# Kernel optimization log

Hardware: AMD Instinct MI355X
Metric: run time of the kernel (lower is better)

The kernel has to match this reference:

```python
import jax, jax.numpy as jnp
import numpy as np

N_NODES = 100000
N_EDGES = 1600000
C = 64          # in = hidden = out channels
L = 3           # num_layers
BN_EPS = 1e-5


def setup_inputs() -> dict:
    key = jax.random.key(0)
    ks = jax.random.split(key, 16)
    x = jax.random.normal(ks[0], (N_NODES, C), dtype=jnp.float32)
    edge_index = jax.random.randint(ks[1], (2, N_EDGES), 0, N_NODES, dtype=jnp.int32)
    s = 1.0 / np.sqrt(C)
    # Stacked per-layer parameters (all layers are C->C).
    # Linear weights stored as [in, out] (i.e. torch weight transposed).
    W1 = jax.random.normal(ks[2], (L, C, C), dtype=jnp.float32) * s
    b1 = jnp.zeros((L, C), dtype=jnp.float32)
    g1 = jnp.ones((L, C), dtype=jnp.float32)    # MLP BN1 gamma
    be1 = jnp.zeros((L, C), dtype=jnp.float32)  # MLP BN1 beta
    W2 = jax.random.normal(ks[3], (L, C, C), dtype=jnp.float32) * s
    b2 = jnp.zeros((L, C), dtype=jnp.float32)
    g2 = jnp.ones((L, C), dtype=jnp.float32)
    be2 = jnp.zeros((L, C), dtype=jnp.float32)
    bn_g = jnp.ones((L, C), dtype=jnp.float32)   # outer per-layer BN gamma
    bn_be = jnp.zeros((L, C), dtype=jnp.float32)
    eps = jnp.zeros((L,), dtype=jnp.float32)     # GIN eps per layer
    return {"x": x, "edge_index": edge_index, "eps": eps,
            "W1": W1, "b1": b1, "g1": g1, "be1": be1,
            "W2": W2, "b2": b2, "g2": g2, "be2": be2,
            "bn_g": bn_g, "bn_be": bn_be}


def _bn(h, g, b):
    # Inference-mode BatchNorm1d with running_mean=0, running_var=1.
    return g * (h * (1.0 / np.sqrt(1.0 + BN_EPS))) + b


def reference(x, edge_index, eps, W1, b1, g1, be1, W2, b2, g2, be2, bn_g, bn_be):
    src, dst = edge_index[0], edge_index[1]
    for i in range(L):
        # GIN message passing: gather source features, scatter-add to targets.
        agg = jax.ops.segment_sum(x[src], dst, num_segments=N_NODES)  # [N, C]
        h = (1.0 + eps[i]) * x + agg
        # 2-layer MLP: Linear -> BN -> ReLU, twice.
        h = jax.nn.relu(_bn(h @ W1[i] + b1[i], g1[i], be1[i]))
        h = jax.nn.relu(_bn(h @ W2[i] + b2[i], g2[i], be2[i]))
        # Outer per-layer BatchNorm.
        x = _bn(h, bn_g[i], bn_be[i])
        if i < L - 1:
            x = jax.nn.relu(x)  # dropout is identity in eval mode
    return x
```

## Files before the change

kernel.cpp:

```cpp
#include <hip/hip_runtime.h>
#include <hip/hip_fp16.h>

#define N_NODES 100000
#define N_EDGES 1600000
#define CH 64
#define NLAYERS 3
#define NBUCKC 98
#define SLABC 18432
#define NFINE (NBUCKC*8)
#define SLABF 2560
#define EPB 4096

typedef _Float16 half8 __attribute__((ext_vector_type(8)));
typedef float floatx4 __attribute__((ext_vector_type(4)));

static __device__ __forceinline__ float4 ld4(const float* p){ return *(const float4*)p; }
static __device__ __forceinline__ unsigned pack2(float a, float b){
  __half2 h = __float22half2_rn(make_float2(a, b));
  return *(unsigned*)&h;
}
static __device__ __forceinline__ half8 ldh8(const unsigned short* p){
  uint4 u = *(const uint4*)p;
  return *(half8*)&u;
}

__global__ __launch_bounds__(256) void part1_kernel(const int* __restrict__ src, const int* __restrict__ dst,
                                                    int* __restrict__ btail, int* __restrict__ pairs){
  __shared__ int lpos[NBUCKC];
  __shared__ int gb[NBUCKC];
  int tid = threadIdx.x;
  if (tid < NBUCKC) lpos[tid] = 0;
  __syncthreads();
  int base = blockIdx.x * EPB;
  int es[EPB/256], ed[EPB/256], er[EPB/256];
  #pragma unroll
  for (int k = 0; k < EPB/256; ++k) {
    int e = base + k*256 + tid;
    if (e < N_EDGES) {
      es[k] = src[e];
      ed[k] = dst[e];
      er[k] = atomicAdd(&lpos[ed[k] >> 10], 1);
    }
  }
  __syncthreads();
  if (tid < NBUCKC) {
    int cc = lpos[tid];
    gb[tid] = cc ? atomicAdd(&btail[tid], cc) : 0;
  }
  __syncthreads();
  #pragma unroll
  for (int k = 0; k < EPB/256; ++k) {
    int e = base + k*256 + tid;
    if (e < N_EDGES) {
      int bk = ed[k] >> 10;
      int idx = gb[bk] + er[k];
      if (idx < (bk+1)*SLABC)
        pairs[idx] = es[k] | ((ed[k] & 1023) << 20);
    }
  }
}

__global__ __launch_bounds__(256) void part2_kernel(const int* __restrict__ pairs, const int* __restrict__ btail,
                                                    int* __restrict__ ftail, int* __restrict__ pairs2){
  __shared__ int cnt[8*32];
  __shared__ int scur[8];
  int tid = threadIdx.x;
  int b = blockIdx.x >> 3;
  int sg = blockIdx.x & 7;
  int e0 = b*SLABC;
  int e1 = btail[b]; int emax = e0 + SLABC; if (e1 > emax) e1 = emax;
  int len = e1 - e0;
  int s0 = e0 + (int)(((long)len * sg) >> 3);
  int s1 = e0 + (int)(((long)len * (sg+1)) >> 3);
  cnt[tid] = 0;
  __syncthreads();
  for (int i = s0 + tid; i < s1; i += 256) {
    int p = pairs[i];
    int fk = ((unsigned)p >> 27);
    atomicAdd(&cnt[(fk<<5) + (tid & 31)], 1);
  }
  __syncthreads();
  if (tid < 8) {
    int tot = 0;
    #pragma unroll
    for (int r = 0; r < 32; ++r) tot += cnt[(tid<<5) + r];
    scur[tid] = tot ? atomicAdd(&ftail[(b<<3) + tid], tot) : 0;
  }
  __syncthreads();
  int lane = tid & 63;
  for (int i = s0 + (tid >> 6)*64; i < s1; i += 256) {
    int my = i + lane;
    bool valid = (my < s1);
    int p = valid ? pairs[my] : 0;
    int fk = valid ? (int)((unsigned)p >> 27) : -1;
    #pragma unroll
    for (int j = 0; j < 8; ++j) {
      unsigned long long mask = __ballot(valid && fk == j);
      if (mask) {
        int leader = __ffsll((long long)mask) - 1;
        int cc = __popcll(mask);
        int basep = 0;
        if (lane == leader) basep = atomicAdd(&scur[j], cc);
        basep = __shfl(basep, leader, 64);
        if (valid && fk == j) {
          int rank = __popcll(mask & ((1ull << lane) - 1ull));
          int pos = basep + rank;
          if (pos < ((b<<3) + j + 1)*SLABF)
            pairs2[pos] = p;
        }
      }
    }
  }
}

__global__ __launch_bounds__(256) void csr_kernel(const int* __restrict__ pairs2, const int* __restrict__ ftail,
                                                  int* __restrict__ offs, int* __restrict__ offe,
                                                  int* __restrict__ srclist){
  __shared__ int c[128];
  __shared__ int s[128];
  __shared__ int cur[128];
  int t = threadIdx.x;
  int f = blockIdx.x;
  int e0 = f*SLABF;
  int e1 = ftail[f]; int emax = e0 + SLABF; if (e1 > emax) e1 = emax;
  if (t < 128) c[t] = 0;
  __syncthreads();
  for (int i = e0 + t; i < e1; i += 256) {
    int p = pairs2[i];
    atomicAdd(&c[((unsigned)p >> 20) & 127], 1);
  }
  __syncthreads();
  int v = (t < 128) ? c[t] : 0;
  if (t < 128) s[t] = v;
  __syncthreads();
  #pragma unroll
  for (int o = 1; o < 128; o <<= 1){
    int u = 0;
    if (t < 128 && t >= o) u = s[t-o];
    __syncthreads();
    if (t < 128) s[t] += u;
    __syncthreads();
  }
  if (t < 128) {
    int excl = s[t] - v;
    cur[t] = excl;
    int n = (f >> 3)*1024 + (f & 7)*128 + t;
    if (n < N_NODES) { offs[n] = e0 + excl; offe[n] = e0 + excl + v; }
  }
  __syncthreads();
  for (int i = e0 + t; i < e1; i += 256) {
    int p = pairs2[i];
    int pos = atomicAdd(&cur[((unsigned)p >> 20) & 127], 1);
    if (pos < SLABF)
      srclist[e0 + pos] = p & 0xFFFFF;
  }
}

__global__ __launch_bounds__(256) void prep_kernel(
    const float* __restrict__ W1, const float* __restrict__ b1,
    const float* __restrict__ g1, const float* __restrict__ be1,
    const float* __restrict__ W2, const float* __restrict__ b2,
    const float* __restrict__ g2, const float* __restrict__ be2,
    const float* __restrict__ bng, const float* __restrict__ bnb,
    _Float16* __restrict__ Wt, float* __restrict__ bf, float* __restrict__ ogb,
    int* __restrict__ btail, int* __restrict__ ftail){
  const float s = 0.9999950000374997f;
  int i = blockIdx.x*256 + threadIdx.x;
  if (i < NBUCKC) btail[i] = i*SLABC;
  if (i < NFINE)  ftail[i] = i*SLABF;
  if (i < NLAYERS*4096) {
    int l = i >> 12, rem = i & 4095, k = rem >> 6, n = rem & 63;
    int di = n*64 + (((k>>3) ^ (n&7))<<3) + (k&7);
    Wt[l*8192 + di]        = (_Float16)(W1[i] * g1[l*64+n] * s);
    Wt[l*8192 + 4096 + di] = (_Float16)(W2[i] * g2[l*64+n] * s);
  }
  if (i < NLAYERS*64) {
    int l = i >> 6, j = i & 63;
    bf[l*128 + j]      = b1[i]*g1[i]*s + be1[i];
    bf[l*128 + 64 + j] = b2[i]*g2[i]*s + be2[i];
    ogb[i]                 = bng[i]*s;
    ogb[NLAYERS*64 + i]    = bnb[i];
  }
}

__global__ __launch_bounds__(256) void xcvt_kernel(const float* __restrict__ x, unsigned short* __restrict__ xb){
  int i = (blockIdx.x*256 + threadIdx.x)*8;
  if (i < N_NODES*CH) {
    float4 v0 = ld4(x + i), v1 = ld4(x + i + 4);
    uint4 w;
    w.x = pack2(v0.x, v0.y); w.y = pack2(v0.z, v0.w);
    w.z = pack2(v1.x, v1.y); w.w = pack2(v1.z, v1.w);
    *(uint4*)(xb + i) = w;
  }
}

__global__ __launch_bounds__(256, 8) void layer_kernel(const unsigned short* __restrict__ XBin,
                                                    const int* __restrict__ offs, const int* __restrict__ offe,
                                                    const int* __restrict__ srclist,
                                                    const float* __restrict__ eps,
                                                    const _Float16* __restrict__ Wt,
                                                    const float* __restrict__ bf, const float* __restrict__ ogb,
                                                    int layer, float* __restrict__ outf,
                                                    _Float16* __restrict__ outb, int relu_out){
  __shared__ _Float16 HsA[64*64];
  __shared__ _Float16 Wts[64*64];
  int tid = threadIdx.x;
  int b = blockIdx.x;
  const _Float16* Wg = Wt + layer*8192;
  *(uint4*)&Wts[tid*8]       = *(const uint4*)&Wg[tid*8];
  *(uint4*)&Wts[(tid+256)*8] = *(const uint4*)&Wg[(tid+256)*8];

  float ep = 1.0f + eps[layer];
  int kb = tid & 7;
  const unsigned short* xr = XBin + (kb << 3);
  #pragma unroll
  for (int p = 0; p < 2; ++p) {
    int nl = p*32 + (tid >> 3);
    int n = b*64 + nl;
    float r[8] = {0,0,0,0,0,0,0,0};
    if (n < N_NODES) {
      half8 A = (half8)(_Float16)0, B = A, C = A, D = A, E = A, F = A, G = A, H = A;
      int e0 = offs[n], e1 = offe[n];
      int e = e0;
      if (e + 8 <= e1) {
        half8 u0 = ldh8(xr + (srclist[e  ]<<6));
        half8 u1 = ldh8(xr + (srclist[e+1]<<6));
        half8 u2 = ldh8(xr + (srclist[e+2]<<6));
        half8 u3 = ldh8(xr + (srclist[e+3]<<6));
        half8 u4 = ldh8(xr + (srclist[e+4]<<6));
        half8 u5 = ldh8(xr + (srclist[e+5]<<6));
        half8 u6 = ldh8(xr + (srclist[e+6]<<6));
        half8 u7 = ldh8(xr + (srclist[e+7]<<6));
        e += 8;
        for (; e + 8 <= e1; e += 8) {
          half8 v0 = ldh8(xr + (srclist[e  ]<<6));
          half8 v1 = ldh8(xr + (srclist[e+1]<<6));
          half8 v2 = ldh8(xr + (srclist[e+2]<<6));
          half8 v3 = ldh8(xr + (srclist[e+3]<<6));
          half8 v4 = ldh8(xr + (srclist[e+4]<<6));
          half8 v5 = ldh8(xr + (srclist[e+5]<<6));
          half8 v6 = ldh8(xr + (srclist[e+6]<<6));
          half8 v7 = ldh8(xr + (srclist[e+7]<<6));
          A += u0; B += u1; C += u2; D += u3;
          E += u4; F += u5; G += u6; H += u7;
          u0 = v0; u1 = v1; u2 = v2; u3 = v3;
          u4 = v4; u5 = v5; u6 = v6; u7 = v7;
        }
        A += u0; B += u1; C += u2; D += u3;
        E += u4; F += u5; G += u6; H += u7;
      }
      for (; e+4 <= e1; e += 4) {
        half8 u0 = ldh8(xr + (srclist[e  ]<<6));
        half8 u1 = ldh8(xr + (srclist[e+1]<<6));
        half8 u2 = ldh8(xr + (srclist[e+2]<<6));
        half8 u3 = ldh8(xr + (srclist[e+3]<<6));
        A += u0; B += u1; C += u2; D += u3;
      }
      for (; e < e1; ++e) {
        A += ldh8(xr + (srclist[e]<<6));
      }
      half8 S = ((A + B) + (C + D)) + ((E + F) + (G + H));
      half8 sv = ldh8(xr + (n<<6));
      #pragma unroll
      for (int i = 0; i < 8; ++i) r[i] = fmaf(ep, (float)sv[i], (float)S[i]);
    }
    uint4 w;
    w.x = pack2(r[0], r[1]); w.y = pack2(r[2], r[3]);
    w.z = pack2(r[4], r[5]); w.w = pack2(r[6], r[7]);
    *(uint4*)&HsA[nl*64 + ((kb ^ (nl&7))<<3)] = w;
  }
  __syncthreads();

  int lane = tid & 63;
  int wid = tid >> 6;
  int c = lane & 15;
  int q = lane >> 4;
  int mbase = wid*16;
  int ma = mbase + c;

  half8 a0 = *(const half8*)&HsA[ma*64 + (((q)   ^ (ma&7))<<3)];
  half8 a1 = *(const half8*)&HsA[ma*64 + (((4+q) ^ (ma&7))<<3)];

  floatx4 acc[4];
  #pragma unroll
  for (int nt = 0; nt < 4; ++nt) {
    int n = nt*16 + c;
    float bv = bf[layer*128 + n];
    floatx4 Acc = {bv, bv, bv, bv};
    half8 b0 = *(const half8*)&Wts[n*64 + (((q)   ^ (n&7))<<3)];
    half8 b1 = *(const half8*)&Wts[n*64 + (((4+q) ^ (n&7))<<3)];
    Acc = __builtin_amdgcn_mfma_f32_16x16x32_f16(a0, b0, Acc, 0, 0, 0);
    Acc = __builtin_amdgcn_mfma_f32_16x16x32_f16(a1, b1, Acc, 0, 0, 0);
    acc[nt] = Acc;
  }
  __syncthreads();

  #pragma unroll
  for (int nt = 0; nt < 4; ++nt) {
    int n = nt*16 + c;
    #pragma unroll
    for (int r = 0; r < 4; ++r) {
      int m = mbase + q*4 + r;
      float h = acc[nt][r]; h = h > 0.f ? h : 0.f;
      HsA[m*64 + (((n>>3) ^ (m&7))<<3) + (n&7)] = (_Float16)h;
    }
  }
  *(uint4*)&Wts[tid*8]       = *(const uint4*)&Wg[4096 + tid*8];
  *(uint4*)&Wts[(tid+256)*8] = *(const uint4*)&Wg[4096 + (tid+256)*8];
  __syncthreads();

  half8 c0 = *(const half8*)&HsA[ma*64 + (((q)   ^ (ma&7))<<3)];
  half8 c1 = *(const half8*)&HsA[ma*64 + (((4+q) ^ (ma&7))<<3)];
  floatx4 acc2[4];
  #pragma unroll
  for (int nt = 0; nt < 4; ++nt) {
    int n = nt*16 + c;
    float bv = bf[layer*128 + 64 + n];
    floatx4 Acc = {bv, bv, bv, bv};
    half8 b0 = *(const half8*)&Wts[n*64 + (((q)   ^ (n&7))<<3)];
    half8 b1 = *(const half8*)&Wts[n*64 + (((4+q) ^ (n&7))<<3)];
    Acc = __builtin_amdgcn_mfma_f32_16x16x32_f16(c0, b0, Acc, 0, 0, 0);
    Acc = __builtin_amdgcn_mfma_f32_16x16x32_f16(c1, b1, Acc, 0, 0, 0);
    acc2[nt] = Acc;
  }

  #pragma unroll
  for (int nt = 0; nt < 4; ++nt) {
    int n = nt*16 + c;
    float og = ogb[layer*64 + n];
    float ob = ogb[NLAYERS*64 + layer*64 + n];
    #pragma unroll
    for (int r = 0; r < 4; ++r) {
      int m = mbase + q*4 + r;
      int gnode = b*64 + m;
      if (gnode < N_NODES) {
        float h = acc2[nt][r]; h = h > 0.f ? h : 0.f;
        float o = fmaf(og, h, ob);
        if (relu_out) {
          o = o > 0.f ? o : 0.f;
          outb[(size_t)gnode*CH + n] = (_Float16)o;
        } else {
          outf[(size_t)gnode*CH + n] = o;
        }
      }
    }
  }
}

extern "C" void kernel_launch(void* const* d_in, const int* in_sizes, int n_in,
                              void* d_out, int out_size, void* d_ws, size_t ws_size,
                              hipStream_t stream) {
  const float* x0  = (const float*)d_in[0];
  const int*   ei  = (const int*)d_in[1];
  const float* eps = (const float*)d_in[2];
  const float* W1  = (const float*)d_in[3];
  const float* b1  = (const float*)d_in[4];
  const float* g1  = (const float*)d_in[5];
  const float* be1 = (const float*)d_in[6];
  const float* W2  = (const float*)d_in[7];
  const float* b2  = (const float*)d_in[8];
  const float* g2  = (const float*)d_in[9];
  const float* be2 = (const float*)d_in[10];
  const float* bng = (const float*)d_in[11];
  const float* bnb = (const float*)d_in[12];
  const int* src = ei;
  const int* dst = ei + N_EDGES;
  float* OUT = (float*)d_out;

  char* p = (char*)d_ws;
  auto carve = [&](size_t bytes)->char*{ char* r = p; p += (bytes + 255) & ~(size_t)255; return r; };
  int*   offs    = (int*)carve((size_t)N_NODES*sizeof(int));
  int*   offe    = (int*)carve((size_t)N_NODES*sizeof(int));
  int*   btail   = (int*)carve(NBUCKC*sizeof(int));
  int*   ftail   = (int*)carve(NFINE*sizeof(int));
  int*   pairs   = (int*)carve((size_t)NBUCKC*SLABC*sizeof(int));
  int*   pairs2  = (int*)carve((size_t)NFINE*SLABF*sizeof(int));
  int*   srclist = (int*)carve((size_t)NFINE*SLABF*sizeof(int));
  unsigned short* XB0 = (unsigned short*)carve((size_t)N_NODES*CH*2);
  unsigned short* XB1 = (unsigned short*)carve((size_t)N_NODES*CH*2);
  _Float16* Wt   = (_Float16*)carve((size_t)NLAYERS*2*4096*2);
  float* bfb     = (float*)carve((size_t)NLAYERS*2*64*sizeof(float));
  float* ogb     = (float*)carve((size_t)2*NLAYERS*64*sizeof(float));

  const int npart = (N_EDGES + EPB - 1)/EPB;
  prep_kernel<<<48, 256, 0, stream>>>(W1,b1,g1,be1,W2,b2,g2,be2,bng,bnb,Wt,bfb,ogb,btail,ftail);
  part1_kernel<<<npart, 256, 0, stream>>>(src, dst, btail, pairs);
  part2_kernel<<<NFINE, 256, 0, stream>>>(pairs, btail, ftail, pairs2);
  csr_kernel<<<NFINE, 256, 0, stream>>>(pairs2, ftail, offs, offe, srclist);
  xcvt_kernel<<<(N_NODES*CH/8 + 255)/256, 256, 0, stream>>>(x0, XB0);

  const int nlb = (N_NODES + 63)/64;
  layer_kernel<<<nlb, 256, 0, stream>>>(XB0, offs, offe, srclist, eps, Wt, bfb, ogb, 0, OUT, (_Float16*)XB1, 1);
  layer_kernel<<<nlb, 256, 0, stream>>>(XB1, offs, offe, srclist, eps, Wt, bfb, ogb, 1, OUT, (_Float16*)XB0, 1);
  layer_kernel<<<nlb, 256, 0, stream>>>(XB0, offs, offe, srclist, eps, Wt, bfb, ogb, 2, OUT, (_Float16*)XB1, 0);
}
```

Measured before the change: 267.7 us.

## Fuse fine-bucket partition into CSR kernel using shared-memory filtering

```diff
diff --git a/kernel.cpp b/kernel.cpp
--- a/kernel.cpp
+++ b/kernel.cpp
@@ -60,74 +60,44 @@
   }
 }
 
-__global__ __launch_bounds__(256) void part2_kernel(const int* __restrict__ pairs, const int* __restrict__ btail,
-                                                    int* __restrict__ ftail, int* __restrict__ pairs2){
-  __shared__ int cnt[8*32];
-  __shared__ int scur[8];
-  int tid = threadIdx.x;
-  int b = blockIdx.x >> 3;
-  int sg = blockIdx.x & 7;
-  int e0 = b*SLABC;
-  int e1 = btail[b]; int emax = e0 + SLABC; if (e1 > emax) e1 = emax;
-  int len = e1 - e0;
-  int s0 = e0 + (int)(((long)len * sg) >> 3);
-  int s1 = e0 + (int)(((long)len * (sg+1)) >> 3);
-  cnt[tid] = 0;
-  __syncthreads();
-  for (int i = s0 + tid; i < s1; i += 256) {
-    int p = pairs[i];
-    int fk = ((unsigned)p >> 27);
-    atomicAdd(&cnt[(fk<<5) + (tid & 31)], 1);
-  }
-  __syncthreads();
-  if (tid < 8) {
-    int tot = 0;
-    #pragma unroll
-    for (int r = 0; r < 32; ++r) tot += cnt[(tid<<5) + r];
-    scur[tid] = tot ? atomicAdd(&ftail[(b<<3) + tid], tot) : 0;
-  }
-  __syncthreads();
-  int lane = tid & 63;
-  for (int i = s0 + (tid >> 6)*64; i < s1; i += 256) {
-    int my = i + lane;
-    bool valid = (my < s1);
-    int p = valid ? pairs[my] : 0;
-    int fk = valid ? (int)((unsigned)p >> 27) : -1;
-    #pragma unroll
-    for (int j = 0; j < 8; ++j) {
-      unsigned long long mask = __ballot(valid && fk == j);
-      if (mask) {
-        int leader = __ffsll((long long)mask) - 1;
-        int cc = __popcll(mask);
-        int basep = 0;
-        if (lane == leader) basep = atomicAdd(&scur[j], cc);
-        basep = __shfl(basep, leader, 64);
-        if (valid && fk == j) {
-          int rank = __popcll(mask & ((1ull << lane) - 1ull));
-          int pos = basep + rank;
-          if (pos < ((b<<3) + j + 1)*SLABF)
-            pairs2[pos] = p;
-        }
-      }
-    }
-  }
-}
-
-__global__ __launch_bounds__(256) void csr_kernel(const int* __restrict__ pairs2, const int* __restrict__ ftail,
-                                                  int* __restrict__ offs, int* __restrict__ offe,
-                                                  int* __restrict__ srclist){
+__global__ __launch_bounds__(256) void csrf_kernel(const int* __restrict__ pairs, const int* __restrict__ btail,
+                                                   int* __restrict__ offs, int* __restrict__ offe,
+                                                   int* __restrict__ srclist){
+  __shared__ int q[SLABF];
+  __shared__ int qn;
   __shared__ int c[128];
   __shared__ int s[128];
   __shared__ int cur[128];
   int t = threadIdx.x;
   int f = blockIdx.x;
-  int e0 = f*SLABF;
-  int e1 = ftail[f]; int emax = e0 + SLABF; if (e1 > emax) e1 = emax;
+  int b = f >> 3;
+  unsigned sub = f & 7;
+  if (t == 0) qn = 0;
   if (t < 128) c[t] = 0;
   __syncthreads();
-  for (int i = e0 + t; i < e1; i += 256) {
-    int p = pairs2[i];
-    atomicAdd(&c[((unsigned)p >> 20) & 127], 1);
+  int e0c = b*SLABC;
+  int e1c = btail[b]; int emax = e0c + SLABC; if (e1c > emax) e1c = emax;
+  int lane = t & 63;
+  for (int ib = e0c; ib < e1c; ib += 256) {
+    int i = ib + t;
+    bool valid = (i < e1c);
+    int p = valid ? pairs[i] : 0;
+    bool m = valid && (((unsigned)p >> 27) == sub);
+    unsigned long long mask = __ballot(m);
+    if (mask) {
+      int leader = __ffsll((long long)mask) - 1;
+      int cnt = __popcll(mask);
+      int basep = 0;
+      if (lane == leader) basep = atomicAdd(&qn, cnt);
+      basep = __shfl(basep, leader, 64);
+      if (m) {
+        int rank = __popcll(mask & ((1ull << lane) - 1ull));
+        int pos = basep + rank;
+        if (pos < SLABF)
+          q[pos] = p;
+        atomicAdd(&c[((unsigned)p >> 20) & 127], 1);
+      }
+    }
   }
   __syncthreads();
   int v = (t < 128) ? c[t] : 0;
@@ -141,6 +111,7 @@
     if (t < 128) s[t] += u;
     __syncthreads();
   }
+  int e0 = f*SLABF;
   if (t < 128) {
     int excl = s[t] - v;
     cur[t] = excl;
@@ -148,8 +119,9 @@
     if (n < N_NODES) { offs[n] = e0 + excl; offe[n] = e0 + excl + v; }
   }
   __syncthreads();
-  for (int i = e0 + t; i < e1; i += 256) {
-    int p = pairs2[i];
+  int qn2 = qn; if (qn2 > SLABF) qn2 = SLABF;
+  for (int i = t; i < qn2; i += 256) {
+    int p = q[i];
     int pos = atomicAdd(&cur[((unsigned)p >> 20) & 127], 1);
     if (pos < SLABF)
       srclist[e0 + pos] = p & 0xFFFFF;
@@ -163,11 +135,10 @@
     const float* __restrict__ g2, const float* __restrict__ be2,
     const float* __restrict__ bng, const float* __restrict__ bnb,
     _Float16* __restrict__ Wt, float* __restrict__ bf, float* __restrict__ ogb,
-    int* __restrict__ btail, int* __restrict__ ftail){
+    int* __restrict__ btail){
   const float s = 0.9999950000374997f;
   int i = blockIdx.x*256 + threadIdx.x;
   if (i < NBUCKC) btail[i] = i*SLABC;
-  if (i < NFINE)  ftail[i] = i*SLABF;
   if (i < NLAYERS*4096) {
     int l = i >> 12, rem = i & 4095, k = rem >> 6, n = rem & 63;
     int di = n*64 + (((k>>3) ^ (n&7))<<3) + (k&7);
@@ -372,9 +343,7 @@
   int*   offs    = (int*)carve((size_t)N_NODES*sizeof(int));
   int*   offe    = (int*)carve((size_t)N_NODES*sizeof(int));
   int*   btail   = (int*)carve(NBUCKC*sizeof(int));
-  int*   ftail   = (int*)carve(NFINE*sizeof(int));
   int*   pairs   = (int*)carve((size_t)NBUCKC*SLABC*sizeof(int));
-  int*   pairs2  = (int*)carve((size_t)NFINE*SLABF*sizeof(int));
   int*   srclist = (int*)carve((size_t)NFINE*SLABF*sizeof(int));
   unsigned short* XB0 = (unsigned short*)carve((size_t)N_NODES*CH*2);
   unsigned short* XB1 = (unsigned short*)carve((size_t)N_NODES*CH*2);
@@ -383,10 +352,9 @@
   float* ogb     = (float*)carve((size_t)2*NLAYERS*64*sizeof(float));
 
   const int npart = (N_EDGES + EPB - 1)/EPB;
-  prep_kernel<<<48, 256, 0, stream>>>(W1,b1,g1,be1,W2,b2,g2,be2,bng,bnb,Wt,bfb,ogb,btail,ftail);
+  prep_kernel<<<48, 256, 0, stream>>>(W1,b1,g1,be1,W2,b2,g2,be2,bng,bnb,Wt,bfb,ogb,btail);
   part1_kernel<<<npart, 256, 0, stream>>>(src, dst, btail, pairs);
-  part2_kernel<<<NFINE, 256, 0, stream>>>(pairs, btail, ftail, pairs2);
-  csr_kernel<<<NFINE, 256, 0, stream>>>(pairs2, ftail, offs, offe, srclist);
+  csrf_kernel<<<NFINE, 256, 0, stream>>>(pairs, btail, offs, offe, srclist);
   xcvt_kernel<<<(N_NODES*CH/8 + 255)/256, 256, 0, stream>>>(x0, XB0);
 
   const int nlb = (N_NODES + 63)/64;
```

Result: slower. 277.1 us (+3.5%).
